# Performance work log

Hardware: AMD Instinct MI355X
Metric: run time of the kernel (lower is better)

The kernel has to match this reference:

```python
import jax, jax.numpy as jnp
import numpy as np

B, H, K, V = 32, 32, 256, 256
CLIP = 1e6


def setup_inputs() -> dict:
    key = jax.random.key(0)
    k1, k2, k3, k4, k5 = jax.random.split(key, 5)
    state = jax.random.normal(k1, (B, H, K, V), dtype=jnp.float32)
    keys = jax.random.normal(k2, (B, H, K), dtype=jnp.float32)
    values = jax.random.normal(k3, (B, H, V), dtype=jnp.float32)
    gates = jax.random.uniform(k4, (B, H, K), dtype=jnp.float32)  # forget gates alpha in (0,1)
    beta = jax.random.uniform(k5, (B, H, 1), dtype=jnp.float32)   # learning rate beta in (0,1)
    return {"state": state, "keys": keys, "values": values, "gates": gates, "beta": beta}


def reference(state, keys, values, gates, beta):
    # KDA delta-rule update: S_t = (I - beta k k^T) Diag(alpha) S_{t-1} + beta k v^T
    state_decayed = gates[..., None] * state                       # (B,H,K,V)
    kt_state = jnp.einsum('bhk,bhkv->bhv', keys, state_decayed)    # k^T (Diag(a) S)
    beta_e = beta[..., None]                                       # (B,H,1,1)
    correction = beta_e * jnp.einsum('bhk,bhv->bhkv', keys, kt_state)
    kv_update = beta_e * jnp.einsum('bhk,bhv->bhkv', keys, values)
    new_state = state_decayed - correction + kv_update
    # NaN -> revert to previous state; Inf -> clip (matches torch module's checks)
    has_nan = jnp.isnan(new_state).any()
    has_inf = jnp.isinf(new_state).any()
    new_state = jnp.where(has_nan, state,
                          jnp.where(has_inf, jnp.clip(new_state, -CLIP, CLIP), new_state))
    return new_state
```

## Files before the change

kernel.cpp:

```cpp
#include <hip/hip_runtime.h>


#define KD 256
#define VD 256

__global__ __launch_bounds__(1024, 4)
void kda_update_kernel(const float* __restrict__ state,
                       const float* __restrict__ keys,
                       const float* __restrict__ values,
                       const float* __restrict__ gates,
                       const float* __restrict__ beta,
                       float* __restrict__ out)
{
    const int bh = blockIdx.x;
    const size_t tile_off = (size_t)bh * (KD * VD);
    const float4* __restrict__ S4 = (const float4*)(state + tile_off);
    float4* __restrict__ O4 = (float4*)(out + tile_off);

    __shared__ float  s_g[KD];
    __shared__ float  s_w[KD];
    __shared__ float  s_c[KD];
    __shared__ float4 s_part[16][64];
    __shared__ float4 s_kt[64];

    const int t = threadIdx.x;
    const int a = t >> 6;
    const int b = t & 63;

    if (t < KD) {
        const float g = gates[bh * KD + t];
        const float k = keys[bh * KD + t];
        s_g[t] = g;
        s_w[t] = g * k;
        s_c[t] = beta[bh] * k;
    }

    float4 s[16];
#pragma unroll
    for (int j = 0; j < 16; ++j) {
        s[j] = S4[t + 1024 * j];
    }

    __syncthreads();

    float4 p = make_float4(0.f, 0.f, 0.f, 0.f);
#pragma unroll
    for (int j = 0; j < 16; ++j) {
        const float w = s_w[a + 16 * j];
        p.x = fmaf(w, s[j].x, p.x);
        p.y = fmaf(w, s[j].y, p.y);
        p.z = fmaf(w, s[j].z, p.z);
        p.w = fmaf(w, s[j].w, p.w);
    }
    s_part[a][b] = p;
    __syncthreads();

    if (t < 64) {
        float4 acc = s_part[0][t];
#pragma unroll
        for (int i = 1; i < 16; ++i) {
            const float4 q = s_part[i][t];
            acc.x += q.x; acc.y += q.y; acc.z += q.z; acc.w += q.w;
        }
        s_kt[t] = acc;
    }
    __syncthreads();

    const float4 kt = s_kt[b];
    const float4 vv = ((const float4*)(values + (size_t)bh * VD))[b];
    const float4 d = make_float4(vv.x - kt.x, vv.y - kt.y, vv.z - kt.z, vv.w - kt.w);

#pragma unroll
    for (int j = 0; j < 16; ++j) {
        const int k = a + 16 * j;
        const float g = s_g[k];
        const float c = s_c[k];
        float4 o;
        o.x = fmaf(g, s[j].x, c * d.x);
        o.y = fmaf(g, s[j].y, c * d.y);
        o.z = fmaf(g, s[j].z, c * d.z);
        o.w = fmaf(g, s[j].w, c * d.w);
        O4[t + 1024 * j] = o;
    }
}

extern "C" void kernel_launch(void* const* d_in, const int* in_sizes, int n_in,
                              void* d_out, int out_size, void* d_ws, size_t ws_size,
                              hipStream_t stream) {
    const float* state  = (const float*)d_in[0];
    const float* keys   = (const float*)d_in[1];
    const float* values = (const float*)d_in[2];
    const float* gates  = (const float*)d_in[3];
    const float* beta   = (const float*)d_in[4];
    float* out = (float*)d_out;

    dim3 grid(32 * 32);
    dim3 block(1024);
    hipLaunchKernelGGL(kda_update_kernel, grid, block, 0, stream,
                       state, keys, values, gates, beta, out);
}
```

Measured before the change: 113.4 us.

## Split each state tile into four column slices across 256-thread blocks with nontemporal access

Each (b,h) tile is now processed by four 256-thread blocks, each owning a 64-column slice, instead of one 1024-thread block, which gives a 4x larger grid of smaller blocks. The column split stays independent because the k^T S reduction runs over rows. State loads and output stores now use nontemporal builtins to avoid polluting caches on this streaming workload. The trade-off is that each slice reads contiguous runs of only 256 bytes per row, and the gate/key vectors are loaded redundantly by all four blocks.

New measurement: 105.7 us. -6.8%, faster.

```diff
diff --git a/kernel.cpp b/kernel.cpp
--- a/kernel.cpp
+++ b/kernel.cpp
@@ -3,8 +3,11 @@
 
 #define KD 256
 #define VD 256
+#define SW 16
 
-__global__ __launch_bounds__(1024, 4)
+typedef float f32x4 __attribute__((ext_vector_type(4)));
+
+__global__ __launch_bounds__(256, 4)
 void kda_update_kernel(const float* __restrict__ state,
                        const float* __restrict__ keys,
                        const float* __restrict__ values,
@@ -12,22 +15,24 @@
                        const float* __restrict__ beta,
                        float* __restrict__ out)
 {
-    const int bh = blockIdx.x;
+    const int bh    = blockIdx.x >> 2;
+    const int slice = blockIdx.x & 3;
     const size_t tile_off = (size_t)bh * (KD * VD);
-    const float4* __restrict__ S4 = (const float4*)(state + tile_off);
-    float4* __restrict__ O4 = (float4*)(out + tile_off);
+    const f32x4* __restrict__ S4 = (const f32x4*)(state + tile_off);
+    f32x4* __restrict__ O4 = (f32x4*)(out + tile_off);
 
-    __shared__ float  s_g[KD];
-    __shared__ float  s_w[KD];
-    __shared__ float  s_c[KD];
-    __shared__ float4 s_part[16][64];
-    __shared__ float4 s_kt[64];
+    __shared__ float s_g[KD];
+    __shared__ float s_w[KD];
+    __shared__ float s_c[KD];
+    __shared__ f32x4 s_part[16][SW];
+    __shared__ f32x4 s_kt[SW];
 
-    const int t = threadIdx.x;
-    const int a = t >> 6;
-    const int b = t & 63;
+    const int t  = threadIdx.x;
+    const int c  = t & (SW - 1);
+    const int r0 = t >> 4;
+    const int c0 = slice * SW;
 
-    if (t < KD) {
+    {
         const float g = gates[bh * KD + t];
         const float k = keys[bh * KD + t];
         s_g[t] = g;
@@ -35,52 +40,53 @@
         s_c[t] = beta[bh] * k;
     }
 
-    float4 s[16];
+    f32x4 s[16];
 #pragma unroll
     for (int j = 0; j < 16; ++j) {
-        s[j] = S4[t + 1024 * j];
+        s[j] = __builtin_nontemporal_load(&S4[(size_t)(r0 + 16 * j) * (VD / 4) + c0 + c]);
     }
 
     __syncthreads();
 
-    float4 p = make_float4(0.f, 0.f, 0.f, 0.f);
+    f32x4 p = (f32x4)(0.f);
 #pragma unroll
     for (int j = 0; j < 16; ++j) {
-        const float w = s_w[a + 16 * j];
+        const float w = s_w[r0 + 16 * j];
         p.x = fmaf(w, s[j].x, p.x);
         p.y = fmaf(w, s[j].y, p.y);
         p.z = fmaf(w, s[j].z, p.z);
         p.w = fmaf(w, s[j].w, p.w);
     }
-    s_part[a][b] = p;
+    s_part[r0][c] = p;
     __syncthreads();
 
-    if (t < 64) {
-        float4 acc = s_part[0][t];
+    if (t < SW) {
+        f32x4 acc = s_part[0][t];
 #pragma unroll
         for (int i = 1; i < 16; ++i) {
-            const float4 q = s_part[i][t];
+            const f32x4 q = s_part[i][t];
             acc.x += q.x; acc.y += q.y; acc.z += q.z; acc.w += q.w;
         }
         s_kt[t] = acc;
     }
     __syncthreads();
 
-    const float4 kt = s_kt[b];
-    const float4 vv = ((const float4*)(values + (size_t)bh * VD))[b];
-    const float4 d = make_float4(vv.x - kt.x, vv.y - kt.y, vv.z - kt.z, vv.w - kt.w);
+    const f32x4 kt = s_kt[c];
+    const f32x4 vv = ((const f32x4*)(values + (size_t)bh * VD))[c0 + c];
+    f32x4 d;
+    d.x = vv.x - kt.x; d.y = vv.y - kt.y; d.z = vv.z - kt.z; d.w = vv.w - kt.w;
 
 #pragma unroll
     for (int j = 0; j < 16; ++j) {
-        const int k = a + 16 * j;
-        const float g = s_g[k];
-        const float c = s_c[k];
-        float4 o;
-        o.x = fmaf(g, s[j].x, c * d.x);
-        o.y = fmaf(g, s[j].y, c * d.y);
-        o.z = fmaf(g, s[j].z, c * d.z);
-        o.w = fmaf(g, s[j].w, c * d.w);
-        O4[t + 1024 * j] = o;
+        const int k = r0 + 16 * j;
+        const float g  = s_g[k];
+        const float cb = s_c[k];
+        f32x4 o;
+        o.x = fmaf(g, s[j].x, cb * d.x);
+        o.y = fmaf(g, s[j].y, cb * d.y);
+        o.z = fmaf(g, s[j].z, cb * d.z);
+        o.w = fmaf(g, s[j].w, cb * d.w);
+        __builtin_nontemporal_store(o, &O4[(size_t)k * (VD / 4) + c0 + c]);
     }
 }
 
@@ -94,8 +100,8 @@
     const float* beta   = (const float*)d_in[4];
     float* out = (float*)d_out;
 
-    dim3 grid(32 * 32);
-    dim3 block(1024);
+    dim3 grid(32 * 32 * 4);
+    dim3 block(256);
     hipLaunchKernelGGL(kda_update_kernel, grid, block, 0, stream,
                        state, keys, values, gates, beta, out);
 }
```
